# Performance work log

Hardware: AMD Instinct MI355X
Metric: run time of the kernel (lower is better)

Reference implementation:

```python
import jax, jax.numpy as jnp
import numpy as np

B, M, H = 4, 128, 1024      # docs, padded mentions per doc, LUKE-large hidden
NH, L = 16, 1024            # attention heads, seq_len
E = 64                      # padded entities per doc
R = 512                     # entity pairs per doc
EMB, BS, NC = 768, 64, 97   # embed_size, block_size, num_class


def setup_inputs() -> dict:
    key = jax.random.key(0)
    ks = jax.random.split(key, 12)
    inp = {
        "seq_lhs": jax.random.normal(ks[0], (B, L, H), jnp.float32),
        "ent_lhs": jax.random.normal(ks[1], (B, M, H), jnp.float32),
        "ent_to_seq_attn": jax.random.uniform(ks[2], (B, NH, M, L), jnp.float32),
        "entity_id_labels": jax.random.randint(ks[3], (B, M), 0, E),
        "hts": jax.random.randint(ks[4], (B, R, 2), 0, E),
        "Wh": jax.random.normal(ks[5], (2 * H, EMB), jnp.float32) * 0.02,
        "bh": jax.random.normal(ks[6], (EMB,), jnp.float32) * 0.02,
        "Wt": jax.random.normal(ks[7], (2 * H, EMB), jnp.float32) * 0.02,
        "bt": jax.random.normal(ks[8], (EMB,), jnp.float32) * 0.02,
        "Wb": jax.random.normal(ks[9], (EMB * BS, NC), jnp.float32) * 0.02,
        "bb": jax.random.normal(ks[10], (NC,), jnp.float32) * 0.02,
    }
    return inp


def reference(seq_lhs, ent_lhs, ent_to_seq_attn, entity_id_labels, hts,
              Wh, bh, Wt, bt, Wb, bb):
    # ---- mention -> entity pooling (segment logsumexp / segment mean) ----
    # global segment id per mention: doc_i * E + entity_label
    ids = (jnp.arange(B)[:, None] * E + entity_id_labels).reshape(-1)  # [B*M]
    m = ent_lhs.reshape(B * M, H)

    seg_max = jax.ops.segment_max(m, ids, num_segments=B * E)          # [B*E, H]
    seg_max = jnp.where(jnp.isfinite(seg_max), seg_max, 0.0)           # empty -> 0
    sumexp = jax.ops.segment_sum(jnp.exp(m - seg_max[ids]), ids, num_segments=B * E)
    cnt = jax.ops.segment_sum(jnp.ones((B * M,), m.dtype), ids, num_segments=B * E)  # [B*E]
    lse = seg_max + jnp.log(jnp.maximum(sumexp, 1e-30))
    ent_embeds = jnp.where(cnt[:, None] > 0, lse, 0.0).reshape(B, E, H)

    # mean of entity-to-seq attention over mentions of each entity
    a = ent_to_seq_attn.transpose(0, 2, 1, 3).reshape(B * M, NH, L)
    a_sum = jax.ops.segment_sum(a, ids, num_segments=B * E)            # [B*E, NH, L]
    ent_attn = (a_sum / jnp.maximum(cnt, 1.0)[:, None, None]).reshape(B, E, NH, L)

    # ---- gather head/tail entities for each pair ----
    h_idx, t_idx = hts[..., 0], hts[..., 1]                            # [B, R]
    hs = jnp.take_along_axis(ent_embeds, h_idx[..., None], axis=1)     # [B, R, H]
    ts = jnp.take_along_axis(ent_embeds, t_idx[..., None], axis=1)
    h_attn = jnp.take_along_axis(ent_attn, h_idx[..., None, None], axis=1)  # [B, R, NH, L]
    t_attn = jnp.take_along_axis(ent_attn, t_idx[..., None, None], axis=1)

    # ---- attn-weighted relation-context embedding ----
    ht_attn = (h_attn * t_attn).mean(axis=2)                           # [B, R, L]
    ht_attn = ht_attn / (ht_attn.sum(-1, keepdims=True) + 1e-5)
    rel = jnp.einsum('bld,brl->brd', seq_lhs, ht_attn)                 # [B, R, H]

    # ---- extractors + block bilinear classifier ----
    hs = jnp.tanh(jnp.concatenate([hs, rel], -1) @ Wh + bh)            # [B, R, EMB]
    ts = jnp.tanh(jnp.concatenate([ts, rel], -1) @ Wt + bt)
    N, K = B * R, EMB // BS
    b1 = hs.reshape(N, K, BS)
    b2 = ts.reshape(N, K, BS)
    bl = (b1[:, :, :, None] * b2[:, :, None, :]).reshape(N, EMB * BS)  # [N, 49152]
    class_logits = bl @ Wb + bb                                        # [N, NC]
    return class_logits
```

## Files before the change

### kernel.cpp

```cpp
#include <hip/hip_runtime.h>
#include <cmath>

#define B_ 4
#define M_ 128
#define H_ 1024
#define NH_ 16
#define L_ 1024
#define E_ 64
#define R_ 512
#define EMB_ 768
#define BS_ 64
#define NC_ 97
#define NPAIR_ (B_*R_)
#define LC_ 16

typedef _Float16 half8 __attribute__((ext_vector_type(8)));
typedef float f32x4 __attribute__((ext_vector_type(4)));

#define OFF_ENT    0
#define OFF_ATTNH  262144
#define OFF_VH     2359296
#define OFF_S      3407872
#define OFF_SEQT   3409920
#define OFF_RELH   5507072
#define OFF_HSF    6555648
#define OFF_TSF    7342080
#define OFF_WHT    8128512
#define OFF_WTT    8914944

__device__ __forceinline__ void gload_lds16(const void* g, void* l) {
    __builtin_amdgcn_global_load_lds(
        (const __attribute__((address_space(1))) unsigned int*)g,
        (__attribute__((address_space(3))) unsigned int*)l, 16, 0, 0);
}

__global__ __launch_bounds__(256) void k_ent_pool(const float* __restrict__ ent_lhs,
                                                  const int* __restrict__ labels,
                                                  float* __restrict__ ent_embeds) {
    int blk = blockIdx.x;
    int b = blk >> 6, e = blk & 63;
    __shared__ int lbl[M_];
    int t = threadIdx.x;
    if (t < M_) lbl[t] = labels[b*M_ + t];
    __syncthreads();
    const float* src = ent_lhs + (size_t)b * M_ * H_;
    float mx[4], sm[4];
    #pragma unroll
    for (int j = 0; j < 4; ++j) { mx[j] = -INFINITY; sm[j] = 0.f; }
    int cnt = 0;
    for (int m = 0; m < M_; ++m) {
        if (lbl[m] != e) continue;
        ++cnt;
        const float* row = src + m * H_;
        #pragma unroll
        for (int j = 0; j < 4; ++j) {
            float x = row[t + j*256];
            if (x > mx[j]) { sm[j] = sm[j] * __expf(mx[j] - x) + 1.f; mx[j] = x; }
            else           { sm[j] += __expf(x - mx[j]); }
        }
    }
    float* dst = ent_embeds + (size_t)blk * H_;
    #pragma unroll
    for (int j = 0; j < 4; ++j)
        dst[t + j*256] = (cnt > 0) ? (mx[j] + __logf(sm[j])) : 0.f;
}

__global__ __launch_bounds__(256) void k_ent_attn(const float* __restrict__ attn,
                                                  const int* __restrict__ labels,
                                                  _Float16* __restrict__ ea_t) {
    int blk = blockIdx.x;
    int b = blk >> 6, e = blk & 63;
    __shared__ int lbl[M_];
    int t = threadIdx.x;
    if (t < M_) lbl[t] = labels[b*M_ + t];
    __syncthreads();
    const float* src = attn + (size_t)b * NH_ * M_ * L_;
    float acc[16][4] = {};
    int cnt = 0;
    for (int m = 0; m < M_; ++m) {
        if (lbl[m] != e) continue;
        ++cnt;
        const float* mp = src + (size_t)m * L_ + t*4;
        #pragma unroll
        for (int nh = 0; nh < 16; ++nh) {
            float4 v = *(const float4*)(mp + (size_t)nh * M_ * L_);
            acc[nh][0] += v.x; acc[nh][1] += v.y; acc[nh][2] += v.z; acc[nh][3] += v.w;
        }
    }
    float inv = 1.f / fmaxf((float)cnt, 1.f);
    _Float16* dst = ea_t + (size_t)blk * L_ * 16;
    #pragma unroll
    for (int j = 0; j < 4; ++j) {
        int l = t*4 + j;
        half8 o0, o1;
        #pragma unroll
        for (int nh = 0; nh < 8; ++nh) { o0[nh] = (_Float16)(acc[nh][j]*inv); o1[nh] = (_Float16)(acc[nh+8][j]*inv); }
        *(half8*)(dst + (size_t)l*16)     = o0;
        *(half8*)(dst + (size_t)l*16 + 8) = o1;
    }
}

__global__ __launch_bounds__(256) void k_ht(const _Float16* __restrict__ ea_t,
                                            const int* __restrict__ hts,
                                            _Float16* __restrict__ vh) {
    int blk = blockIdx.x;
    int b = blk >> 6, lc = blk & 63;
    int l0 = lc * LC_;
    __shared__ _Float16 tile[64*256];
    int t = threadIdx.x;
    {
        int e = t >> 2, part = t & 3;
        const _Float16* src = ea_t + ((size_t)(b*64 + e)*L_ + l0) * 16;
        #pragma unroll
        for (int u = 0; u < 8; ++u) {
            int unit = part*8 + u;
            int l = unit >> 1, nhh = unit & 1;
            half8 v = *(const half8*)(src + l*16 + nhh*8);
            *(half8*)&tile[e*256 + ((l ^ (e & 15))*16) + nhh*8] = v;
        }
    }
    __syncthreads();
    const int* hp = hts + b * R_ * 2;
    #pragma unroll
    for (int pp = 0; pp < 2; ++pp) {
        int p = pp*256 + t;
        int he = hp[p*2], te = hp[p*2 + 1];
        const _Float16* ha = &tile[he*256];
        const _Float16* ta = &tile[te*256];
        float accl[LC_];
        #pragma unroll
        for (int l = 0; l < LC_; ++l) {
            half8 h0 = *(const half8*)&ha[((l ^ (he & 15))*16)];
            half8 h1 = *(const half8*)&ha[((l ^ (he & 15))*16) + 8];
            half8 t0 = *(const half8*)&ta[((l ^ (te & 15))*16)];
            half8 t1 = *(const half8*)&ta[((l ^ (te & 15))*16) + 8];
            float s = 0.f;
            #pragma unroll
            for (int q = 0; q < 8; ++q)
                s += (float)h0[q]*(float)t0[q] + (float)h1[q]*(float)t1[q];
            accl[l] = s;
        }
        half8 o0, o1;
        #pragma unroll
        for (int q = 0; q < 8; ++q) { o0[q] = (_Float16)accl[q]; o1[q] = (_Float16)accl[q+8]; }
        _Float16* dst = vh + (size_t)(b*R_ + p)*L_ + l0;
        *(half8*)dst = o0;
        *(half8*)(dst + 8) = o1;
    }
}

__global__ __launch_bounds__(256) void k_rowsum(const _Float16* __restrict__ vh,
                                                float* __restrict__ s) {
    int row = blockIdx.x*4 + (threadIdx.x >> 6);
    int lane = threadIdx.x & 63;
    const _Float16* r = vh + (size_t)row * L_;
    float acc = 0.f;
    #pragma unroll
    for (int u = 0; u < 2; ++u) {
        half8 v = *(const half8*)(r + (lane + u*64)*8);
        #pragma unroll
        for (int q = 0; q < 8; ++q) acc += (float)v[q];
    }
    #pragma unroll
    for (int off = 32; off > 0; off >>= 1) acc += __shfl_down(acc, off);
    if (lane == 0) s[row] = acc;
}

__global__ __launch_bounds__(256) void k_prep_seqt(const float* __restrict__ seq,
                                                   _Float16* __restrict__ seqT) {
    int l0 = blockIdx.x*64, d0 = blockIdx.y*64, b = blockIdx.z;
    __shared__ _Float16 sl[64*72];
    int t = threadIdx.x;
    int lr = t >> 4, dc = (t & 15)*4;
    #pragma unroll
    for (int u = 0; u < 4; ++u) {
        int l = lr + u*16;
        float4 v = *(const float4*)(seq + ((size_t)(b*L_ + l0 + l))*H_ + d0 + dc);
        sl[l*72 + dc+0] = (_Float16)v.x; sl[l*72 + dc+1] = (_Float16)v.y;
        sl[l*72 + dc+2] = (_Float16)v.z; sl[l*72 + dc+3] = (_Float16)v.w;
    }
    __syncthreads();
    int d = t >> 2, lo = (t & 3)*16;
    half8 o0, o1;
    #pragma unroll
    for (int q = 0; q < 8; ++q) { o0[q] = sl[(lo+q)*72 + d]; o1[q] = sl[(lo+8+q)*72 + d]; }
    _Float16* dst = seqT + ((size_t)(b*H_ + d0 + d))*L_ + l0 + lo;
    *(half8*)dst = o0;
    *(half8*)(dst + 8) = o1;
}

__global__ __launch_bounds__(256) void k_prep_wt(const float* __restrict__ W,
                                                 _Float16* __restrict__ WT) {
    int k0 = blockIdx.x * 64;
    int d0 = blockIdx.y * 64;
    __shared__ float s[64*65];
    int t = threadIdx.x;
    #pragma unroll
    for (int u = 0; u < 16; ++u) {
        int idx = t + u*256; int rr = idx >> 6, cc = idx & 63;
        s[rr*65 + cc] = W[(size_t)(k0+rr)*EMB_ + d0 + cc];
    }
    __syncthreads();
    #pragma unroll
    for (int u = 0; u < 16; ++u) {
        int idx = t + u*256; int dd = idx >> 6, kk = idx & 63;
        WT[(size_t)(d0+dd)*2048 + k0 + kk] = (_Float16)s[kk*65 + dd];
    }
}

__global__ __launch_bounds__(256) void k_prep_wbt(const float* __restrict__ Wb,
                                                  _Float16* __restrict__ Wbt) {
    int kbi = blockIdx.x;
    __shared__ float s[64*97];
    int t = threadIdx.x;
    size_t gbase = (size_t)kbi * 64 * NC_;
    #pragma unroll
    for (int u = 0; u < 25; ++u) {
        int idx = t + u*256;
        if (idx < 64*NC_) s[idx] = Wb[gbase + idx];
    }
    __syncthreads();
    _Float16* dst = Wbt + (size_t)kbi * 112*64;
    #pragma unroll
    for (int u = 0; u < 28; ++u) {
        int idx = t + u*256;
        int c = idx >> 6, j = idx & 63;
        float v = (c < NC_) ? s[j*NC_ + c] : 0.f;
        dst[idx] = (_Float16)v;
    }
}

__global__ __launch_bounds__(256) void k_rel_mfma(const _Float16* __restrict__ vh,
                                                  const _Float16* __restrict__ seqT,
                                                  const float* __restrict__ s,
                                                  _Float16* __restrict__ relh) {
    const int d0 = blockIdx.x * 64;
    const int n0 = blockIdx.y * 64;
    const int b  = n0 >> 9;
    __shared__ _Float16 bs[2][64*64];
    const int t = threadIdx.x;
    const int w = t >> 6, lane = t & 63;
    const int r = lane & 15, g = lane >> 4;
    const int row8 = lane >> 3, u8 = lane & 7;
    const int swz_w = (u8 ^ row8) * 8;

    const _Float16* bsrc = seqT + ((size_t)(b*H_) + d0) * L_;
    #pragma unroll
    for (int c2 = w*2; c2 < w*2+2; ++c2)
        gload_lds16(bsrc + (size_t)(c2*8 + row8)*L_ + swz_w, &bs[0][c2*512]);

    const _Float16* ap = vh + (size_t)(n0 + w*16 + r) * L_;
    half8 nA0 = *(const half8*)(ap + g*8);
    half8 nA1 = *(const half8*)(ap + 32 + g*8);

    f32x4 acc[4] = {};
    __syncthreads();

    for (int c = 0; c < 16; ++c) {
        const int cur = c & 1;
        if (c < 15) {
            const int k0n = (c+1)*64;
            #pragma unroll
            for (int c2 = w*2; c2 < w*2+2; ++c2)
                gload_lds16(bsrc + (size_t)(c2*8 + row8)*L_ + k0n + swz_w, &bs[cur^1][c2*512]);
        }
        half8 cA0 = nA0, cA1 = nA1;
        if (c < 15) {
            const int k0n = (c+1)*64;
            nA0 = *(const half8*)(ap + k0n + g*8);
            nA1 = *(const half8*)(ap + k0n + 32 + g*8);
        }
        #pragma unroll
        for (int df = 0; df < 4; ++df) {
            half8 b0 = *(const half8*)&bs[cur][(df*16 + r)*64 + ((g ^ (r&7))*8)];
            acc[df] = __builtin_amdgcn_mfma_f32_16x16x32_f16(cA0, b0, acc[df], 0, 0, 0);
            half8 b1 = *(const half8*)&bs[cur][(df*16 + r)*64 + (((4+g) ^ (r&7))*8)];
            acc[df] = __builtin_amdgcn_mfma_f32_16x16x32_f16(cA1, b1, acc[df], 0, 0, 0);
        }
        __syncthreads();
    }
    const int nb = n0 + w*16 + g*4;
    float invs[4];
    #pragma unroll
    for (int q = 0; q < 4; ++q) invs[q] = 1.f / (s[nb + q] + 1.6e-4f);
    #pragma unroll
    for (int df = 0; df < 4; ++df)
        #pragma unroll
        for (int q = 0; q < 4; ++q)
            relh[(size_t)(nb + q)*H_ + d0 + df*16 + r] = (_Float16)(acc[df][q] * invs[q]);
}

__global__ __launch_bounds__(256) void k_extract_mfma(const float* __restrict__ ent_embeds,
                                                      const _Float16* __restrict__ relh,
                                                      const int* __restrict__ hts,
                                                      const _Float16* __restrict__ WhT,
                                                      const _Float16* __restrict__ WtT,
                                                      const float* __restrict__ bh,
                                                      const float* __restrict__ bt,
                                                      _Float16* __restrict__ hsf,
                                                      _Float16* __restrict__ tsf) {
    const int which = blockIdx.z;
    const _Float16* WT = which ? WtT : WhT;
    const float* bias  = which ? bt : bh;
    _Float16* outh     = which ? tsf : hsf;

    const int d0 = blockIdx.x * 64;
    const int n0 = blockIdx.y * 64;
    __shared__ _Float16 wt_s[2][64*64];
    const int t = threadIdx.x;
    const int w = t >> 6, lane = t & 63;
    const int r = lane & 15, g = lane >> 4;
    const int row8 = lane >> 3, u8 = lane & 7;
    const int swz_w = (u8 ^ row8) * 8;

    const int nrow = n0 + w*16 + r;
    const int hidx = hts[nrow*2 + which];
    const float* entp = ent_embeds + ((size_t)((nrow >> 9)*E_ + hidx))*H_;
    const _Float16* relp = relh + (size_t)nrow * H_;

    #pragma unroll
    for (int c2 = w*2; c2 < w*2+2; ++c2)
        gload_lds16(WT + (size_t)(d0 + c2*8 + row8)*2048 + swz_w, &wt_s[0][c2*512]);

    float4 nF0 = *(const float4*)(entp + g*8);
    float4 nF1 = *(const float4*)(entp + g*8 + 4);
    float4 nF2 = *(const float4*)(entp + 32 + g*8);
    float4 nF3 = *(const float4*)(entp + 32 + g*8 + 4);
    half8 nH0 = {}, nH1 = {};

    f32x4 acc[4] = {};
    __syncthreads();

    for (int c = 0; c < 32; ++c) {
        const int cur = c & 1;
        if (c < 31) {
            const int k0n = (c+1)*64;
            #pragma unroll
            for (int c2 = w*2; c2 < w*2+2; ++c2)
                gload_lds16(WT + (size_t)(d0 + c2*8 + row8)*2048 + k0n + swz_w,
                            &wt_s[cur^1][c2*512]);
        }
        half8 aF0, aF1;
        if (c < 16) {
            aF0 = half8{ (_Float16)nF0.x, (_Float16)nF0.y, (_Float16)nF0.z, (_Float16)nF0.w,
                         (_Float16)nF1.x, (_Float16)nF1.y, (_Float16)nF1.z, (_Float16)nF1.w };
            aF1 = half8{ (_Float16)nF2.x, (_Float16)nF2.y, (_Float16)nF2.z, (_Float16)nF2.w,
                         (_Float16)nF3.x, (_Float16)nF3.y, (_Float16)nF3.z, (_Float16)nF3.w };
        } else {
            aF0 = nH0; aF1 = nH1;
        }
        if (c < 31) {
            const int k0n = (c+1)*64;
            if (k0n < 1024) {
                const float* ar = entp + k0n;
                nF0 = *(const float4*)(ar + g*8);
                nF1 = *(const float4*)(ar + g*8 + 4);
                nF2 = *(const float4*)(ar + 32 + g*8);
                nF3 = *(const float4*)(ar + 32 + g*8 + 4);
            } else {
                const _Float16* ar = relp + (k0n - 1024);
                nH0 = *(const half8*)(ar + g*8);
                nH1 = *(const half8*)(ar + 32 + g*8);
            }
        }
        #pragma unroll
        for (int df = 0; df < 4; ++df) {
            half8 b0 = *(const half8*)&wt_s[cur][(df*16 + r)*64 + ((g ^ (r&7))*8)];
            acc[df] = __builtin_amdgcn_mfma_f32_16x16x32_f16(aF0, b0, acc[df], 0, 0, 0);
            half8 b1 = *(const half8*)&wt_s[cur][(df*16 + r)*64 + (((4+g) ^ (r&7))*8)];
            acc[df] = __builtin_amdgcn_mfma_f32_16x16x32_f16(aF1, b1, acc[df], 0, 0, 0);
        }
        __syncthreads();
    }
    #pragma unroll
    for (int df = 0; df < 4; ++df) {
        float bv = bias[d0 + df*16 + r];
        #pragma unroll
        for (int q2 = 0; q2 < 4; ++q2) {
            float v = tanhf(acc[df][q2] + bv);
            outh[(size_t)(n0 + w*16 + g*4 + q2)*EMB_ + d0 + df*16 + r] = (_Float16)v;
        }
    }
}

__global__ void k_init_out(const float* __restrict__ bb, float* __restrict__ out) {
    int idx = blockIdx.x*256 + threadIdx.x;
    if (idx < NPAIR_*NC_) out[idx] = bb[idx % NC_];
}

__global__ __launch_bounds__(256) void k_cls_mfma(const _Float16* __restrict__ hsf,
                                                  const _Float16* __restrict__ tsf,
                                                  const _Float16* __restrict__ Wbt,
                                                  float* __restrict__ out) {
    const int kb2 = blockIdx.x;
    const int kb = kb2 >> 1, ih = kb2 & 1;
    const int n0 = blockIdx.y * 64;
    __shared__ _Float16 ts_s[64*72];
    __shared__ _Float16 hs_s[64*40];
    __shared__ _Float16 wb_s[2][112*64];
    const int t = threadIdx.x;
    const int w = t >> 6, lane = t & 63;
    const int r = lane & 15, g = lane >> 4;
    const int row8 = lane >> 3, u8 = lane & 7;
    const int swz_w = (u8 ^ row8) * 8;

    {
        int n = t & 63, q = t >> 6;
        const half8 tv0 = *(const half8*)&tsf[(size_t)(n0+n)*EMB_ + kb*64 + q*16];
        const half8 tv1 = *(const half8*)&tsf[(size_t)(n0+n)*EMB_ + kb*64 + q*16 + 8];
        *(half8*)&ts_s[n*72 + q*16]     = tv0;
        *(half8*)&ts_s[n*72 + q*16 + 8] = tv1;
        const half8 hv = *(const half8*)&hsf[(size_t)(n0+n)*EMB_ + kb*64 + ih*32 + q*8];
        *(half8*)&hs_s[n*40 + q*8] = hv;
    }
    const _Float16* wsrc = Wbt + (size_t)(kb*64 + ih*32) * 7168;
    for (int c = w; c < 14; c += 4)
        gload_lds16(wsrc + (c*8 + row8)*64 + swz_w, &wb_s[0][c*512]);

    __syncthreads();

    const half8 tsF0 = *(const half8*)&ts_s[(w*16 + r)*72 + g*8];
    const half8 tsF1 = *(const half8*)&ts_s[(w*16 + r)*72 + 32 + g*8];

    f32x4 acc[7] = {};
    for (int i = 0; i < 32; ++i) {
        const int cur = i & 1;
        if (i < 31) {
            const _Float16* sp = wsrc + (size_t)(i+1) * 7168;
            for (int c = w; c < 14; c += 4)
                gload_lds16(sp + (c*8 + row8)*64 + swz_w, &wb_s[cur^1][c*512]);
        }
        _Float16 h = hs_s[(w*16 + r)*40 + i];
        half8 a0, a1;
        #pragma unroll
        for (int e = 0; e < 8; ++e) { a0[e] = tsF0[e] * h; a1[e] = tsF1[e] * h; }
        #pragma unroll
        for (int cf = 0; cf < 7; ++cf) {
            half8 b0 = *(const half8*)&wb_s[cur][(cf*16 + r)*64 + ((g ^ (r&7))*8)];
            acc[cf] = __builtin_amdgcn_mfma_f32_16x16x32_f16(a0, b0, acc[cf], 0, 0, 0);
            half8 b1 = *(const half8*)&wb_s[cur][(cf*16 + r)*64 + (((4+g) ^ (r&7))*8)];
            acc[cf] = __builtin_amdgcn_mfma_f32_16x16x32_f16(a1, b1, acc[cf], 0, 0, 0);
        }
        __syncthreads();
    }
    #pragma unroll
    for (int cf = 0; cf < 7; ++cf) {
        int c = cf*16 + r;
        #pragma unroll
        for (int q2 = 0; q2 < 4; ++q2) {
            if (cf < 6 || r == 0)
                atomicAdd(&out[(size_t)(n0 + w*16 + g*4 + q2)*NC_ + c], acc[cf][q2]);
        }
    }
}

extern "C" void kernel_launch(void* const* d_in, const int* in_sizes, int n_in,
                              void* d_out, int out_size, void* d_ws, size_t ws_size,
                              hipStream_t stream) {
    (void)in_sizes; (void)n_in; (void)out_size; (void)ws_size;
    const float* seq  = (const float*)d_in[0];
    const float* ent  = (const float*)d_in[1];
    const float* attn = (const float*)d_in[2];
    const int*   lbl  = (const int*)d_in[3];
    const int*   hts  = (const int*)d_in[4];
    const float* Wh   = (const float*)d_in[5];
    const float* bh   = (const float*)d_in[6];
    const float* Wt   = (const float*)d_in[7];
    const float* bt   = (const float*)d_in[8];
    const float* Wb   = (const float*)d_in[9];
    const float* bb   = (const float*)d_in[10];
    float* out = (float*)d_out;
    float* ws  = (float*)d_ws;

    float*    ent_embeds = ws + OFF_ENT;
    _Float16* ea_t = (_Float16*)(ws + OFF_ATTNH);
    _Float16* vh   = (_Float16*)(ws + OFF_VH);
    float*    sv   = ws + OFF_S;
    _Float16* seqT = (_Float16*)(ws + OFF_SEQT);
    _Float16* relh = (_Float16*)(ws + OFF_RELH);
    _Float16* hsf  = (_Float16*)(ws + OFF_HSF);
    _Float16* tsf  = (_Float16*)(ws + OFF_TSF);
    _Float16* WhT  = (_Float16*)(ws + OFF_WHT);
    _Float16* WtT  = (_Float16*)(ws + OFF_WTT);
    _Float16* Wbt  = (_Float16*)(ws + OFF_ATTNH);

    k_prep_seqt<<<dim3(16, 16, 4), 256, 0, stream>>>(seq, seqT);
    k_prep_wt<<<dim3(32, 12), 256, 0, stream>>>(Wh, WhT);
    k_prep_wt<<<dim3(32, 12), 256, 0, stream>>>(Wt, WtT);
    k_ent_pool<<<B_*E_, 256, 0, stream>>>(ent, lbl, ent_embeds);
    k_ent_attn<<<B_*E_, 256, 0, stream>>>(attn, lbl, ea_t);
    k_ht<<<B_*64, 256, 0, stream>>>(ea_t, hts, vh);
    k_rowsum<<<NPAIR_/4, 256, 0, stream>>>(vh, sv);
    k_rel_mfma<<<dim3(16, 32), 256, 0, stream>>>(vh, seqT, sv, relh);
    k_prep_wbt<<<768, 256, 0, stream>>>(Wb, Wbt);
    k_extract_mfma<<<dim3(12, 32, 2), 256, 0, stream>>>(ent_embeds, relh, hts, WhT, WtT, bh, bt, hsf, tsf);
    k_init_out<<<(NPAIR_*NC_ + 255)/256, 256, 0, stream>>>(bb, out);
    k_cls_mfma<<<dim3(24, 32), 256, 0, stream>>>(hsf, tsf, Wbt, out);
}
```

Baseline: 302.3 us.

## Restructure bilinear classifier GEMM with larger pair tiles and deterministic split-K reduce

The classifier kernel now tiles 128 pairs per block and covers a full 64-wide head block per block, holding the tail-embedding fragments in registers and reading Wb fragments straight from global memory instead of double-buffering them through LDS. Each K-block writes partial logits to a workspace buffer, and a separate reduce kernel sums the 12 partials and adds the bias, replacing the init kernel and the atomicAdd accumulation. Wb padding grows from 112 to 128 classes so each wave handles 32 classes. The intent is more reuse of each Wb fragment across pairs and no atomic contention. The cost is fewer blocks (192), heavier register use, and uncached global B-fragment loads.

```diff
diff --git a/kernel.cpp b/kernel.cpp
--- a/kernel.cpp
+++ b/kernel.cpp
@@ -220,9 +220,9 @@
         if (idx < 64*NC_) s[idx] = Wb[gbase + idx];
     }
     __syncthreads();
-    _Float16* dst = Wbt + (size_t)kbi * 112*64;
-    #pragma unroll
-    for (int u = 0; u < 28; ++u) {
+    _Float16* dst = Wbt + (size_t)kbi * 8192;
+    #pragma unroll
+    for (int u = 0; u < 32; ++u) {
         int idx = t + u*256;
         int c = idx >> 6, j = idx & 63;
         float v = (c < NC_) ? s[j*NC_ + c] : 0.f;
@@ -383,75 +383,84 @@
     }
 }
 
-__global__ void k_init_out(const float* __restrict__ bb, float* __restrict__ out) {
-    int idx = blockIdx.x*256 + threadIdx.x;
-    if (idx < NPAIR_*NC_) out[idx] = bb[idx % NC_];
-}
-
 __global__ __launch_bounds__(256) void k_cls_mfma(const _Float16* __restrict__ hsf,
                                                   const _Float16* __restrict__ tsf,
                                                   const _Float16* __restrict__ Wbt,
-                                                  float* __restrict__ out) {
-    const int kb2 = blockIdx.x;
-    const int kb = kb2 >> 1, ih = kb2 & 1;
-    const int n0 = blockIdx.y * 64;
-    __shared__ _Float16 ts_s[64*72];
-    __shared__ _Float16 hs_s[64*40];
-    __shared__ _Float16 wb_s[2][112*64];
+                                                  float* __restrict__ partial) {
+    const int kb = blockIdx.x;
+    const int n0 = blockIdx.y * 128;
     const int t = threadIdx.x;
     const int w = t >> 6, lane = t & 63;
     const int r = lane & 15, g = lane >> 4;
-    const int row8 = lane >> 3, u8 = lane & 7;
-    const int swz_w = (u8 ^ row8) * 8;
+    __shared__ _Float16 hs_s[128*72];
 
     {
-        int n = t & 63, q = t >> 6;
-        const half8 tv0 = *(const half8*)&tsf[(size_t)(n0+n)*EMB_ + kb*64 + q*16];
-        const half8 tv1 = *(const half8*)&tsf[(size_t)(n0+n)*EMB_ + kb*64 + q*16 + 8];
-        *(half8*)&ts_s[n*72 + q*16]     = tv0;
-        *(half8*)&ts_s[n*72 + q*16 + 8] = tv1;
-        const half8 hv = *(const half8*)&hsf[(size_t)(n0+n)*EMB_ + kb*64 + ih*32 + q*8];
-        *(half8*)&hs_s[n*40 + q*8] = hv;
-    }
-    const _Float16* wsrc = Wbt + (size_t)(kb*64 + ih*32) * 7168;
-    for (int c = w; c < 14; c += 4)
-        gload_lds16(wsrc + (c*8 + row8)*64 + swz_w, &wb_s[0][c*512]);
-
-    __syncthreads();
-
-    const half8 tsF0 = *(const half8*)&ts_s[(w*16 + r)*72 + g*8];
-    const half8 tsF1 = *(const half8*)&ts_s[(w*16 + r)*72 + 32 + g*8];
-
-    f32x4 acc[7] = {};
-    for (int i = 0; i < 32; ++i) {
-        const int cur = i & 1;
-        if (i < 31) {
-            const _Float16* sp = wsrc + (size_t)(i+1) * 7168;
-            for (int c = w; c < 14; c += 4)
-                gload_lds16(sp + (c*8 + row8)*64 + swz_w, &wb_s[cur^1][c*512]);
-        }
-        _Float16 h = hs_s[(w*16 + r)*40 + i];
-        half8 a0, a1;
-        #pragma unroll
-        for (int e = 0; e < 8; ++e) { a0[e] = tsF0[e] * h; a1[e] = tsF1[e] * h; }
-        #pragma unroll
-        for (int cf = 0; cf < 7; ++cf) {
-            half8 b0 = *(const half8*)&wb_s[cur][(cf*16 + r)*64 + ((g ^ (r&7))*8)];
-            acc[cf] = __builtin_amdgcn_mfma_f32_16x16x32_f16(a0, b0, acc[cf], 0, 0, 0);
-            half8 b1 = *(const half8*)&wb_s[cur][(cf*16 + r)*64 + (((4+g) ^ (r&7))*8)];
-            acc[cf] = __builtin_amdgcn_mfma_f32_16x16x32_f16(a1, b1, acc[cf], 0, 0, 0);
-        }
-        __syncthreads();
-    }
-    #pragma unroll
-    for (int cf = 0; cf < 7; ++cf) {
-        int c = cf*16 + r;
-        #pragma unroll
-        for (int q2 = 0; q2 < 4; ++q2) {
-            if (cf < 6 || r == 0)
-                atomicAdd(&out[(size_t)(n0 + w*16 + g*4 + q2)*NC_ + c], acc[cf][q2]);
-        }
-    }
+        int n = t & 127, hh = t >> 7;
+        const _Float16* src = &hsf[(size_t)(n0+n)*EMB_ + kb*64 + hh*32];
+        #pragma unroll
+        for (int u = 0; u < 4; ++u)
+            *(half8*)&hs_s[n*72 + hh*32 + u*8] = *(const half8*)(src + u*8);
+    }
+    half8 tsF[8][2];
+    #pragma unroll
+    for (int nf = 0; nf < 8; ++nf) {
+        const _Float16* tp = &tsf[(size_t)(n0 + nf*16 + r)*EMB_ + kb*64];
+        tsF[nf][0] = *(const half8*)(tp + g*8);
+        tsF[nf][1] = *(const half8*)(tp + 32 + g*8);
+    }
+    __syncthreads();
+
+    const _Float16* wb = Wbt + (size_t)(kb*64) * 8192;
+    f32x4 acc[8][2] = {};
+
+    #pragma unroll 2
+    for (int i = 0; i < 64; ++i) {
+        const _Float16* ws_ = wb + (size_t)i * 8192;
+        half8 b00, b01, b10, b11;
+        {
+            const _Float16* bp0 = ws_ + (size_t)(w*32 + r)*64;
+            const _Float16* bp1 = ws_ + (size_t)(w*32 + 16 + r)*64;
+            b00 = *(const half8*)(bp0 + g*8);
+            b01 = *(const half8*)(bp0 + 32 + g*8);
+            b10 = *(const half8*)(bp1 + g*8);
+            b11 = *(const half8*)(bp1 + 32 + g*8);
+        }
+        #pragma unroll
+        for (int nf = 0; nf < 8; ++nf) {
+            _Float16 h = hs_s[(nf*16 + r)*72 + i];
+            half8 a0, a1;
+            #pragma unroll
+            for (int e = 0; e < 8; ++e) { a0[e] = tsF[nf][0][e] * h; a1[e] = tsF[nf][1][e] * h; }
+            acc[nf][0] = __builtin_amdgcn_mfma_f32_16x16x32_f16(a0, b00, acc[nf][0], 0, 0, 0);
+            acc[nf][0] = __builtin_amdgcn_mfma_f32_16x16x32_f16(a1, b01, acc[nf][0], 0, 0, 0);
+            acc[nf][1] = __builtin_amdgcn_mfma_f32_16x16x32_f16(a0, b10, acc[nf][1], 0, 0, 0);
+            acc[nf][1] = __builtin_amdgcn_mfma_f32_16x16x32_f16(a1, b11, acc[nf][1], 0, 0, 0);
+        }
+    }
+    float* pdst = partial + (size_t)kb * 2048 * 128;
+    #pragma unroll
+    for (int nf = 0; nf < 8; ++nf) {
+        #pragma unroll
+        for (int cl = 0; cl < 2; ++cl) {
+            int c = w*32 + cl*16 + r;
+            #pragma unroll
+            for (int q = 0; q < 4; ++q)
+                pdst[(size_t)(n0 + nf*16 + g*4 + q)*128 + c] = acc[nf][cl][q];
+        }
+    }
+}
+
+__global__ __launch_bounds__(256) void k_reduce(const float* __restrict__ partial,
+                                                const float* __restrict__ bb,
+                                                float* __restrict__ out) {
+    int idx = blockIdx.x*256 + threadIdx.x;
+    if (idx >= NPAIR_*NC_) return;
+    int n = idx / NC_, c = idx - n*NC_;
+    float s = bb[c];
+    #pragma unroll
+    for (int kb = 0; kb < 12; ++kb)
+        s += partial[((size_t)kb*2048 + n)*128 + c];
+    out[idx] = s;
 }
 
 extern "C" void kernel_launch(void* const* d_in, const int* in_sizes, int n_in,
@@ -483,6 +492,7 @@
     _Float16* WhT  = (_Float16*)(ws + OFF_WHT);
     _Float16* WtT  = (_Float16*)(ws + OFF_WTT);
     _Float16* Wbt  = (_Float16*)(ws + OFF_ATTNH);
+    float*    part = ws + OFF_SEQT;
 
     k_prep_seqt<<<dim3(16, 16, 4), 256, 0, stream>>>(seq, seqT);
     k_prep_wt<<<dim3(32, 12), 256, 0, stream>>>(Wh, WhT);
@@ -494,6 +504,6 @@
     k_rel_mfma<<<dim3(16, 32), 256, 0, stream>>>(vh, seqT, sv, relh);
     k_prep_wbt<<<768, 256, 0, stream>>>(Wb, Wbt);
     k_extract_mfma<<<dim3(12, 32, 2), 256, 0, stream>>>(ent_embeds, relh, hts, WhT, WtT, bh, bt, hsf, tsf);
-    k_init_out<<<(NPAIR_*NC_ + 255)/256, 256, 0, stream>>>(bb, out);
-    k_cls_mfma<<<dim3(24, 32), 256, 0, stream>>>(hsf, tsf, Wbt, out);
-}
+    k_cls_mfma<<<dim3(12, 16), 256, 0, stream>>>(hsf, tsf, Wbt, part);
+    k_reduce<<<(NPAIR_*NC_ + 255)/256, 256, 0, stream>>>(part, bb, out);
+}
```

After: 292.6 us. 1.03x faster.
